# Kernel optimization log

Hardware: AMD Instinct MI355X
Metric: run time of the kernel (lower is better)

Reference implementation:

```python
import jax, jax.numpy as jnp
import numpy as np

H, X, Y = 64, 4, 2
B, N = 64, 4096

def _mlp2(x, W1, b1, W2, b2):
    # GraphEncoderMLP: Linear -> ReLU -> Linear -> ReLU (pointwise over last dim)
    return jax.nn.relu(jnp.dot(jax.nn.relu(jnp.dot(x, W1) + b1), W2) + b2)

def _t(a):
    return jnp.transpose(a, (0, 2, 1))

def _forward(hx, past_curr_mess, fut_curr_mess, y_curr_mess, hy,
             pc_W1, pc_b1, pc_W2, pc_b2,
             fc_W1, fc_b1, fc_W2, fc_b2,
             yc_W1, yc_b1, yc_W2, yc_b2,
             nd_W1, nd_b1, nd_W2, nd_b2,
             W_ih, b_ih, W_hh, b_hh,
             dec_W1, dec_b1, dec_W2, dec_b2):
    # hx: [B, H, N]; messages: [B, X, N]; hy: [B, H, N]
    hx_past = jnp.concatenate([hx[:, :, :1], hx[:, :, :-1]], axis=2)
    hx_fut = jnp.concatenate([hx[:, :, 1:], hx[:, :, -1:]], axis=2)
    pc_in = _t(jnp.concatenate([hx_past, hx, past_curr_mess], axis=1))  # [B,N,2H+X]
    fc_in = _t(jnp.concatenate([hx_fut, hx, fut_curr_mess], axis=1))
    yc_in = _t(jnp.concatenate([hy, hx, y_curr_mess], axis=1))
    pe = _mlp2(pc_in, pc_W1, pc_b1, pc_W2, pc_b2)  # [B,N,H]
    fe = _mlp2(fc_in, fc_W1, fc_b1, fc_W2, fc_b2)
    ye = _mlp2(yc_in, yc_W1, yc_b1, yc_W2, yc_b2)
    U = _mlp2(pe + fe + ye, nd_W1, nd_b1, nd_W2, nd_b2)  # [B,N,H]
    hprev = _t(hx)  # [B,N,H]
    gi = jnp.dot(U, W_ih) + b_ih          # [B,N,3H]
    gh = jnp.dot(hprev, W_hh) + b_hh
    ir, iz, ig = jnp.split(gi, 3, axis=-1)
    hr, hz, hg = jnp.split(gh, 3, axis=-1)
    r = jax.nn.sigmoid(ir + hr)
    z = jax.nn.sigmoid(iz + hz)
    n = jnp.tanh(ig + r * hg)
    hnew = (1.0 - z) * n + z * hprev      # [B,N,H]
    # GraphDecoder: pointwise Linear -> ReLU -> Linear to x_dim
    eps = jnp.dot(jax.nn.relu(jnp.dot(hnew, dec_W1) + dec_b1), dec_W2) + dec_b2  # [B,N,X]
    return _t(eps), _t(hnew)  # ([B,X,N], [B,H,N])

def setup_inputs() -> dict:
    key = jax.random.key(0)
    ks = jax.random.split(key, 40)
    s = 0.05
    d = {
        'hx': jax.random.normal(ks[0], (B, H, N), jnp.float32),
        'past_curr_mess': jax.random.normal(ks[1], (B, X, N), jnp.float32),
        'fut_curr_mess': jax.random.normal(ks[2], (B, X, N), jnp.float32),
        'y_curr_mess': jax.random.normal(ks[3], (B, X, N), jnp.float32),
        'hy': jax.random.normal(ks[4], (B, H, N), jnp.float32),
    }
    i = 5
    for name in ['pc', 'fc', 'yc']:
        d[name + '_W1'] = jax.random.normal(ks[i], (2 * H + X, H), jnp.float32) * s; i += 1
        d[name + '_b1'] = jnp.zeros((H,), jnp.float32)
        d[name + '_W2'] = jax.random.normal(ks[i], (H, H), jnp.float32) * s; i += 1
        d[name + '_b2'] = jnp.zeros((H,), jnp.float32)
    d['nd_W1'] = jax.random.normal(ks[i], (H, H), jnp.float32) * s; i += 1
    d['nd_b1'] = jnp.zeros((H,), jnp.float32)
    d['nd_W2'] = jax.random.normal(ks[i], (H, H), jnp.float32) * s; i += 1
    d['nd_b2'] = jnp.zeros((H,), jnp.float32)
    d['W_ih'] = jax.random.normal(ks[i], (H, 3 * H), jnp.float32) * s; i += 1
    d['b_ih'] = jnp.zeros((3 * H,), jnp.float32)
    d['W_hh'] = jax.random.normal(ks[i], (H, 3 * H), jnp.float32) * s; i += 1
    d['b_hh'] = jnp.zeros((3 * H,), jnp.float32)
    d['dec_W1'] = jax.random.normal(ks[i], (H, H), jnp.float32) * s; i += 1
    d['dec_b1'] = jnp.zeros((H,), jnp.float32)
    d['dec_W2'] = jax.random.normal(ks[i], (H, X), jnp.float32) * s; i += 1
    d['dec_b2'] = jnp.zeros((X,), jnp.float32)
    return d

def reference(hx, past_curr_mess, fut_curr_mess, y_curr_mess, hy,
              pc_W1, pc_b1, pc_W2, pc_b2,
              fc_W1, fc_b1, fc_W2, fc_b2,
              yc_W1, yc_b1, yc_W2, yc_b2,
              nd_W1, nd_b1, nd_W2, nd_b2,
              W_ih, b_ih, W_hh, b_hh,
              dec_W1, dec_b1, dec_W2, dec_b2):
    return _forward(hx, past_curr_mess, fut_curr_mess, y_curr_mess, hy,
                    pc_W1, pc_b1, pc_W2, pc_b2,
                    fc_W1, fc_b1, fc_W2, fc_b2,
                    yc_W1, yc_b1, yc_W2, yc_b2,
                    nd_W1, nd_b1, nd_W2, nd_b2,
                    W_ih, b_ih, W_hh, b_hh,
                    dec_W1, dec_b1, dec_W2, dec_b2)
```

## Files before the change

### kernel.cpp

```cpp
#include <hip/hip_runtime.h>

#define NPOS 4096
#define NB   64

typedef __bf16 bf8v __attribute__((ext_vector_type(8)));
typedef float  f4   __attribute__((ext_vector_type(4)));

__device__ __forceinline__ float sigm(float x)   { return 1.0f / (1.0f + __expf(-x)); }
__device__ __forceinline__ float tanh_f(float x) { return 1.0f - 2.0f / (1.0f + __expf(2.0f * x)); }

__device__ __forceinline__ f4 MF(bf8v a, bf8v b, f4 c) {
    return __builtin_amdgcn_mfma_f32_16x16x32_bf16(a, b, c, 0, 0, 0);
}

__device__ __forceinline__ void gl_lds16(const void* g, void* l) {
    __builtin_amdgcn_global_load_lds(
        (const __attribute__((address_space(1))) void*)g,
        (__attribute__((address_space(3)))       void*)l,
        16, 0, 0);
}

#define NFRAG 211

__global__ __launch_bounds__(64) void prep_kernel(
    const float* __restrict__ pcW1, const float* __restrict__ pcb1, const float* __restrict__ pcW2, const float* __restrict__ pcb2,
    const float* __restrict__ fcW1, const float* __restrict__ fcb1, const float* __restrict__ fcW2, const float* __restrict__ fcb2,
    const float* __restrict__ ycW1, const float* __restrict__ ycb1, const float* __restrict__ ycW2, const float* __restrict__ ycb2,
    const float* __restrict__ ndW1, const float* __restrict__ ndb1, const float* __restrict__ ndW2, const float* __restrict__ ndb2,
    const float* __restrict__ Wih,  const float* __restrict__ bih,  const float* __restrict__ Whh,  const float* __restrict__ bhh,
    const float* __restrict__ dW1,  const float* __restrict__ db1,  const float* __restrict__ dW2,  const float* __restrict__ db2,
    char* __restrict__ ws)
{
    const int f = blockIdx.x, l = threadIdx.x;
    const int sg = l >> 4, c16 = l & 15;
    char* dst = ws + (size_t)f * 1024 + (size_t)l * 16;

    int kind = 0;
    const float* W = nullptr; const float* B1 = nullptr; const float* B2 = nullptr;
    int t = 0, kb = 0, ncol = 64, coloff = 0, boff = 0, mlp = 0;
    bool msgmask = false, decw2 = false, db2frag = false, perm = false;

    if (f < 108) {
        const int m = f / 36, r = f % 36;
        const float* W1 = (m == 0 ? pcW1 : (m == 1 ? fcW1 : ycW1));
        const float* W2 = (m == 0 ? pcW2 : (m == 1 ? fcW2 : ycW2));
        const float* b1 = (m == 0 ? pcb1 : (m == 1 ? fcb1 : ycb1));
        const float* b2 = (m == 0 ? pcb2 : (m == 1 ? fcb2 : ycb2));
        if (r < 20)      { W = W1; kb = r >> 2; t = r & 3; msgmask = (kb == 4); mlp = m; }
        else if (r < 28) { W = W2; int rr = r - 20; kb = rr >> 2; t = rr & 3; perm = true; }
        else if (r < 32) { kind = 1; B1 = b1; t = r - 28; }
        else             { kind = 1; B1 = b2; t = r - 32; }
    } else if (f < 132) {
        const int r = f - 108;
        if (r < 8)       { W = ndW1; kb = r >> 2; t = r & 3; perm = true; }
        else if (r < 16) { W = ndW2; int rr = r - 8; kb = rr >> 2; t = rr & 3; perm = true; }
        else if (r < 20) { kind = 1; B1 = ndb1; t = r - 16; }
        else             { kind = 1; B1 = ndb2; t = r - 20; }
    } else if (f < 164) {
        const int r = f - 132; ncol = 192;
        if (r < 8)       { W = Whh; coloff = 128; kb = r >> 2; t = r & 3; }
        else if (r < 16) { W = Wih; coloff = 0;   int rr = r - 8;  kb = rr >> 2; t = rr & 3; perm = true; }
        else if (r < 24) { W = Whh; coloff = 0;   int rr = r - 16; kb = rr >> 2; t = rr & 3; }
        else if (r < 28) { kind = 1; B1 = bhh; boff = 128; t = r - 24; }
        else             { kind = 1; B1 = bih; B2 = bhh; boff = 0; t = r - 28; }
    } else if (f < 196) {
        const int r = f - 164; ncol = 192;
        if (r < 8)       { W = Wih; coloff = 128; kb = r >> 2; t = r & 3; perm = true; }
        else if (r < 16) { W = Wih; coloff = 64;  int rr = r - 8;  kb = rr >> 2; t = rr & 3; perm = true; }
        else if (r < 24) { W = Whh; coloff = 64;  int rr = r - 16; kb = rr >> 2; t = rr & 3; }
        else if (r < 28) { kind = 1; B1 = bih; boff = 128; t = r - 24; }
        else             { kind = 1; B1 = bih; B2 = bhh; boff = 64; t = r - 28; }
    } else {
        const int r = f - 196;
        if (r < 8)       { W = dW1; kb = r >> 2; t = r & 3; perm = true; }
        else if (r < 10) { W = dW2; kb = r - 8; t = 0; decw2 = true; perm = true; }
        else if (r < 14) { kind = 1; B1 = db1; t = r - 10; }
        else             { kind = 1; B1 = db2; t = 0; db2frag = true; }
    }

    if (!kind) {
        const int row = 16 * t + c16;
        bf8v v;
        #pragma unroll
        for (int j = 0; j < 8; ++j) {
            const int k = perm ? (kb * 32 + 16 * (j >> 2) + 4 * sg + (j & 3))
                               : (kb * 32 + sg * 8 + j);
            float x;
            if (msgmask) { const int kk = k - 128 - mlp * 4; x = (kk >= 0 && kk < 4) ? W[(128 + kk) * 64 + row] : 0.f; }
            else if (decw2) { x = (row < 4) ? W[k * 4 + row] : 0.f; }
            else { x = W[k * ncol + coloff + row]; }
            v[j] = (__bf16)x;
        }
        *(bf8v*)dst = v;
    } else {
        f4 o;
        #pragma unroll
        for (int r4 = 0; r4 < 4; ++r4) {
            float x;
            if (db2frag) { x = (sg == 0 && t == 0) ? B1[r4] : 0.f; }
            else {
                const int fi = boff + 16 * t + 4 * sg + r4;
                x = B1[fi]; if (B2) x += B2[fi];
            }
            o[r4] = x;
        }
        *(f4*)dst = o;
    }
}

#define WSTRIDE 36864
#define LDSZ    73728

__global__ __launch_bounds__(256, 2) void kgnn_main(
    const float* __restrict__ hx,  const float* __restrict__ pcm,
    const float* __restrict__ fcm, const float* __restrict__ ycm,
    const float* __restrict__ hy,
    const char*  __restrict__ ws,  float* __restrict__ out)
{
    __shared__ __align__(16) char LD[LDSZ];
    char* const bufA = LD;
    char* const bufB = LD + WSTRIDE;
    const int tid  = threadIdx.x;
    const int b    = blockIdx.x >> 5;
    const int tile = blockIdx.x & 31;
    const int n0   = tile * 128;
    const int baseH = b * 64 * NPOS;
    const int baseX = b * 4 * NPOS;

    const int lane = tid & 63, wid = tid >> 6;
    const int s = lane >> 4, q = lane & 15;
    const int Pv[2] = { wid * 32 + q, wid * 32 + 16 + q };
    const int Gn[2] = { n0 + Pv[0], n0 + Pv[1] };

    auto ldTB = [&](const float* __restrict__ T, int gnq, int h) -> bf8v {
        bf8v v;
        #pragma unroll
        for (int j = 0; j < 8; ++j)
            v[j] = (__bf16)T[baseH + (h * 32 + 8 * s + j) * NPOS + gnq];
        return v;
    };
    auto packB = [&](const f4* aa, int h, bool relu) -> bf8v {
        bf8v v;
        #pragma unroll
        for (int j = 0; j < 8; ++j) {
            float x = aa[2 * h + (j >> 2)][j & 3];
            if (relu) x = fmaxf(x, 0.f);
            v[j] = (__bf16)x;
        }
        return v;
    };

    bf8v hxn0[2], hxn1[2], msgB[2];
    #pragma unroll
    for (int cc = 0; cc < 2; ++cc) {
        hxn0[cc] = ldTB(hx, Gn[cc], 0);
        hxn1[cc] = ldTB(hx, Gn[cc], 1);
        #pragma unroll
        for (int j = 0; j < 8; ++j) {
            const int idx = 8 * s + j;
            float x = 0.f;
            if      (idx < 4)  x = pcm[baseX + idx * NPOS + Gn[cc]];
            else if (idx < 8)  x = fcm[baseX + (idx - 4) * NPOS + Gn[cc]];
            else if (idx < 12) x = ycm[baseX + (idx - 8) * NPOS + Gn[cc]];
            msgB[cc][j] = (__bf16)x;
        }
    }

    auto stageA = [&](char* dstbuf, int gbase, int nf) {
        #pragma unroll
        for (int f0 = 0; f0 < 9; ++f0) {
            const int f = f0 * 4 + wid;
            if (f < nf)
                gl_lds16(ws + ((size_t)(gbase + f) << 10) + ((size_t)lane << 4),
                         dstbuf + (f << 10));
        }
    };

    auto ldAL = [&](const char* base, int fl) -> bf8v {
        return *(const bf8v*)(base + (fl << 10) + (lane << 4));
    };
    auto ldBiasL = [&](const char* base, int fl) -> f4 {
        return *(const f4*)(base + (fl << 10) + (lane << 4));
    };

    stageA(bufA, 0, 36);
    __syncthreads();

    bf8v sB[2][2];
    #pragma unroll
    for (int m = 0; m < 3; ++m) {
        char* cur = (m & 1) ? bufB : bufA;
        char* oth = (m & 1) ? bufA : bufB;
        stageA(oth, (m == 0) ? 36 : (m == 1 ? 72 : 108), (m == 2) ? 24 : 36);

        bf8v e0[2], e1[2];
        #pragma unroll
        for (int cc = 0; cc < 2; ++cc) {
            if (m == 0) {
                const int gm = (Gn[cc] == 0) ? 0 : Gn[cc] - 1;
                e0[cc] = ldTB(hx, gm, 0); e1[cc] = ldTB(hx, gm, 1);
            } else if (m == 1) {
                const int gp = (Gn[cc] == NPOS - 1) ? NPOS - 1 : Gn[cc] + 1;
                e0[cc] = ldTB(hx, gp, 0); e1[cc] = ldTB(hx, gp, 1);
            } else {
                e0[cc] = ldTB(hy, Gn[cc], 0); e1[cc] = ldTB(hy, Gn[cc], 1);
            }
        }
        f4 a[2][4];
        #pragma unroll
        for (int t = 0; t < 4; ++t) { f4 bv = ldBiasL(cur, 28 + t); a[0][t] = bv; a[1][t] = bv; }
        #pragma unroll
        for (int t = 0; t < 4; ++t) { bf8v A = ldAL(cur, t);      a[0][t] = MF(A, e0[0],   a[0][t]); a[1][t] = MF(A, e0[1],   a[1][t]); }
        #pragma unroll
        for (int t = 0; t < 4; ++t) { bf8v A = ldAL(cur, 4 + t);  a[0][t] = MF(A, e1[0],   a[0][t]); a[1][t] = MF(A, e1[1],   a[1][t]); }
        #pragma unroll
        for (int t = 0; t < 4; ++t) { bf8v A = ldAL(cur, 8 + t);  a[0][t] = MF(A, hxn0[0], a[0][t]); a[1][t] = MF(A, hxn0[1], a[1][t]); }
        #pragma unroll
        for (int t = 0; t < 4; ++t) { bf8v A = ldAL(cur, 12 + t); a[0][t] = MF(A, hxn1[0], a[0][t]); a[1][t] = MF(A, hxn1[1], a[1][t]); }
        #pragma unroll
        for (int t = 0; t < 4; ++t) { bf8v A = ldAL(cur, 16 + t); a[0][t] = MF(A, msgB[0], a[0][t]); a[1][t] = MF(A, msgB[1], a[1][t]); }

        bf8v u0[2] = { packB(a[0], 0, true), packB(a[1], 0, true) };
        bf8v u1[2] = { packB(a[0], 1, true), packB(a[1], 1, true) };

        f4 a2[2][4];
        #pragma unroll
        for (int t = 0; t < 4; ++t) { f4 bv = ldBiasL(cur, 32 + t); a2[0][t] = bv; a2[1][t] = bv; }
        #pragma unroll
        for (int t = 0; t < 4; ++t) { bf8v A = ldAL(cur, 20 + t); a2[0][t] = MF(A, u0[0], a2[0][t]); a2[1][t] = MF(A, u0[1], a2[1][t]); }
        #pragma unroll
        for (int t = 0; t < 4; ++t) { bf8v A = ldAL(cur, 24 + t); a2[0][t] = MF(A, u1[0], a2[0][t]); a2[1][t] = MF(A, u1[1], a2[1][t]); }
        #pragma unroll
        for (int cc = 0; cc < 2; ++cc)
            #pragma unroll
            for (int h = 0; h < 2; ++h) {
                bf8v p = packB(a2[cc], h, true);
                if (m == 0) sB[cc][h] = p;
                else {
                    #pragma unroll
                    for (int j = 0; j < 8; ++j)
                        sB[cc][h][j] = (__bf16)((float)sB[cc][h][j] + (float)p[j]);
                }
            }
        __syncthreads();
    }

    bf8v uu0[2], uu1[2];
    {
        stageA(bufA, 132, 32);
        f4 a[2][4];
        #pragma unroll
        for (int t = 0; t < 4; ++t) { f4 bv = ldBiasL(bufB, 16 + t); a[0][t] = bv; a[1][t] = bv; }
        #pragma unroll
        for (int t = 0; t < 4; ++t) { bf8v A = ldAL(bufB, t);     a[0][t] = MF(A, sB[0][0], a[0][t]); a[1][t] = MF(A, sB[1][0], a[1][t]); }
        #pragma unroll
        for (int t = 0; t < 4; ++t) { bf8v A = ldAL(bufB, 4 + t); a[0][t] = MF(A, sB[0][1], a[0][t]); a[1][t] = MF(A, sB[1][1], a[1][t]); }
        bf8v w0[2] = { packB(a[0], 0, true), packB(a[1], 0, true) };
        bf8v w1[2] = { packB(a[0], 1, true), packB(a[1], 1, true) };
        f4 a2[2][4];
        #pragma unroll
        for (int t = 0; t < 4; ++t) { f4 bv = ldBiasL(bufB, 20 + t); a2[0][t] = bv; a2[1][t] = bv; }
        #pragma unroll
        for (int t = 0; t < 4; ++t) { bf8v A = ldAL(bufB, 8 + t);  a2[0][t] = MF(A, w0[0], a2[0][t]); a2[1][t] = MF(A, w0[1], a2[1][t]); }
        #pragma unroll
        for (int t = 0; t < 4; ++t) { bf8v A = ldAL(bufB, 12 + t); a2[0][t] = MF(A, w1[0], a2[0][t]); a2[1][t] = MF(A, w1[1], a2[1][t]); }
        uu0[0] = packB(a2[0], 0, true); uu0[1] = packB(a2[1], 0, true);
        uu1[0] = packB(a2[0], 1, true); uu1[1] = packB(a2[1], 1, true);
        __syncthreads();
    }

    bf8v gB[2][2];
    {
        stageA(bufB, 164, 32);
        f4 g0[2][4];
        #pragma unroll
        for (int t = 0; t < 4; ++t) { f4 bv = ldBiasL(bufA, 24 + t); g0[0][t] = bv; g0[1][t] = bv; }
        #pragma unroll
        for (int t = 0; t < 4; ++t) { bf8v A = ldAL(bufA, t);     g0[0][t] = MF(A, hxn0[0], g0[0][t]); g0[1][t] = MF(A, hxn0[1], g0[1][t]); }
        #pragma unroll
        for (int t = 0; t < 4; ++t) { bf8v A = ldAL(bufA, 4 + t); g0[0][t] = MF(A, hxn1[0], g0[0][t]); g0[1][t] = MF(A, hxn1[1], g0[1][t]); }
        f4 rr[2][4];
        #pragma unroll
        for (int t = 0; t < 4; ++t) { f4 bv = ldBiasL(bufA, 28 + t); rr[0][t] = bv; rr[1][t] = bv; }
        #pragma unroll
        for (int t = 0; t < 4; ++t) { bf8v A = ldAL(bufA, 8 + t);  rr[0][t] = MF(A, uu0[0], rr[0][t]); rr[1][t] = MF(A, uu0[1], rr[1][t]); }
        #pragma unroll
        for (int t = 0; t < 4; ++t) { bf8v A = ldAL(bufA, 12 + t); rr[0][t] = MF(A, uu1[0], rr[0][t]); rr[1][t] = MF(A, uu1[1], rr[1][t]); }
        #pragma unroll
        for (int t = 0; t < 4; ++t) { bf8v A = ldAL(bufA, 16 + t); rr[0][t] = MF(A, hxn0[0], rr[0][t]); rr[1][t] = MF(A, hxn0[1], rr[1][t]); }
        #pragma unroll
        for (int t = 0; t < 4; ++t) { bf8v A = ldAL(bufA, 20 + t); rr[0][t] = MF(A, hxn1[0], rr[0][t]); rr[1][t] = MF(A, hxn1[1], rr[1][t]); }
        #pragma unroll
        for (int cc = 0; cc < 2; ++cc)
            #pragma unroll
            for (int t = 0; t < 4; ++t)
                #pragma unroll
                for (int r = 0; r < 4; ++r)
                    gB[cc][t >> 1][(t & 1) * 4 + r] = (__bf16)(sigm(rr[cc][t][r]) * g0[cc][t][r]);
        __syncthreads();
    }

    bf8v hnB0[2], hnB1[2];
    {
        stageA(bufA, 196, 15);
        f4 gi[2][4];
        #pragma unroll
        for (int t = 0; t < 4; ++t) { f4 bv = ldBiasL(bufB, 24 + t); gi[0][t] = bv; gi[1][t] = bv; }
        #pragma unroll
        for (int t = 0; t < 4; ++t) { bf8v A = ldAL(bufB, t);     gi[0][t] = MF(A, uu0[0], gi[0][t]); gi[1][t] = MF(A, uu0[1], gi[1][t]); }
        #pragma unroll
        for (int t = 0; t < 4; ++t) { bf8v A = ldAL(bufB, 4 + t); gi[0][t] = MF(A, uu1[0], gi[0][t]); gi[1][t] = MF(A, uu1[1], gi[1][t]); }
        bf8v nB[2][2];
        #pragma unroll
        for (int cc = 0; cc < 2; ++cc)
            #pragma unroll
            for (int t = 0; t < 4; ++t)
                #pragma unroll
                for (int r = 0; r < 4; ++r)
                    nB[cc][t >> 1][(t & 1) * 4 + r] =
                        (__bf16)tanh_f(gi[cc][t][r] + (float)gB[cc][t >> 1][(t & 1) * 4 + r]);

        f4 hpv[2][4];
        #pragma unroll
        for (int cc = 0; cc < 2; ++cc)
            #pragma unroll
            for (int t = 0; t < 4; ++t)
                #pragma unroll
                for (int r = 0; r < 4; ++r)
                    hpv[cc][t][r] = hx[baseH + (16 * t + 4 * s + r) * NPOS + Gn[cc]];

        f4 zz[2][4];
        #pragma unroll
        for (int t = 0; t < 4; ++t) { f4 bv = ldBiasL(bufB, 28 + t); zz[0][t] = bv; zz[1][t] = bv; }
        #pragma unroll
        for (int t = 0; t < 4; ++t) { bf8v A = ldAL(bufB, 8 + t);  zz[0][t] = MF(A, uu0[0], zz[0][t]); zz[1][t] = MF(A, uu0[1], zz[1][t]); }
        #pragma unroll
        for (int t = 0; t < 4; ++t) { bf8v A = ldAL(bufB, 12 + t); zz[0][t] = MF(A, uu1[0], zz[0][t]); zz[1][t] = MF(A, uu1[1], zz[1][t]); }
        #pragma unroll
        for (int t = 0; t < 4; ++t) { bf8v A = ldAL(bufB, 16 + t); zz[0][t] = MF(A, hxn0[0], zz[0][t]); zz[1][t] = MF(A, hxn0[1], zz[1][t]); }
        #pragma unroll
        for (int t = 0; t < 4; ++t) { bf8v A = ldAL(bufB, 20 + t); zz[0][t] = MF(A, hxn1[0], zz[0][t]); zz[1][t] = MF(A, hxn1[1], zz[1][t]); }

        float* __restrict__ outH = out + NB * 4 * NPOS + baseH;
        #pragma unroll
        for (int cc = 0; cc < 2; ++cc)
            #pragma unroll
            for (int t = 0; t < 4; ++t)
                #pragma unroll
                for (int r = 0; r < 4; ++r) {
                    float z  = sigm(zz[cc][t][r]);
                    float nn = (float)nB[cc][t >> 1][(t & 1) * 4 + r];
                    float hv = nn + z * (hpv[cc][t][r] - nn);
                    outH[(16 * t + 4 * s + r) * NPOS + Gn[cc]] = hv;
                    if (t < 2) hnB0[cc][(t & 1) * 4 + r] = (__bf16)hv;
                    else       hnB1[cc][(t & 1) * 4 + r] = (__bf16)hv;
                }
        __syncthreads();
    }

    {
        f4 a[2][4];
        #pragma unroll
        for (int t = 0; t < 4; ++t) { f4 bv = ldBiasL(bufA, 10 + t); a[0][t] = bv; a[1][t] = bv; }
        #pragma unroll
        for (int t = 0; t < 4; ++t) { bf8v A = ldAL(bufA, t);     a[0][t] = MF(A, hnB0[0], a[0][t]); a[1][t] = MF(A, hnB0[1], a[1][t]); }
        #pragma unroll
        for (int t = 0; t < 4; ++t) { bf8v A = ldAL(bufA, 4 + t); a[0][t] = MF(A, hnB1[0], a[0][t]); a[1][t] = MF(A, hnB1[1], a[1][t]); }
        bf8v e0[2] = { packB(a[0], 0, true), packB(a[1], 0, true) };
        bf8v e1[2] = { packB(a[0], 1, true), packB(a[1], 1, true) };
        f4 ep[2];
        { f4 bv = ldBiasL(bufA, 14); ep[0] = bv; ep[1] = bv; }
        { bf8v A = ldAL(bufA, 8); ep[0] = MF(A, e0[0], ep[0]); ep[1] = MF(A, e0[1], ep[1]); }
        { bf8v A = ldAL(bufA, 9); ep[0] = MF(A, e1[0], ep[0]); ep[1] = MF(A, e1[1], ep[1]); }
        if (s == 0) {
            #pragma unroll
            for (int cc = 0; cc < 2; ++cc) {
                #pragma unroll
                for (int r = 0; r < 4; ++r) out[baseX + r * NPOS + Gn[cc]] = ep[cc][r];
            }
        }
    }
}

extern "C" void kernel_launch(void* const* d_in, const int* in_sizes, int n_in,
                              void* d_out, int out_size, void* d_ws, size_t ws_size,
                              hipStream_t stream) {
    const float* hx   = (const float*)d_in[0];
    const float* pcm  = (const float*)d_in[1];
    const float* fcm  = (const float*)d_in[2];
    const float* ycm  = (const float*)d_in[3];
    const float* hy   = (const float*)d_in[4];

    prep_kernel<<<dim3(NFRAG), dim3(64), 0, stream>>>(
        (const float*)d_in[5],  (const float*)d_in[6],  (const float*)d_in[7],  (const float*)d_in[8],
        (const float*)d_in[9],  (const float*)d_in[10], (const float*)d_in[11], (const float*)d_in[12],
        (const float*)d_in[13], (const float*)d_in[14], (const float*)d_in[15], (const float*)d_in[16],
        (const float*)d_in[17], (const float*)d_in[18], (const float*)d_in[19], (const float*)d_in[20],
        (const float*)d_in[21], (const float*)d_in[22], (const float*)d_in[23], (const float*)d_in[24],
        (const float*)d_in[25], (const float*)d_in[26], (const float*)d_in[27], (const float*)d_in[28],
        (char*)d_ws);

    kgnn_main<<<dim3(NB * 32), dim3(256), 0, stream>>>(
        hx, pcm, fcm, ycm, hy, (const char*)d_ws, (float*)d_out);
}
```

Baseline: 100.4 us.

## Split block work across 8 waves with one 16-column chunk per wave

Each block now launches 512 threads (8 waves) instead of 256, and each wave handles a single 16-position column group instead of two. This halves per-thread register state (accumulators, B fragments) and doubles the waves available for latency hiding, while the LDS weight staging is spread across 8 waves. Each weight fragment loaded from LDS now feeds only one MFMA instead of two, so LDS read traffic per MFMA doubles. The launch bounds request 4 blocks per CU, which the 72KB of LDS per block may not permit.

```diff
diff --git a/kernel.cpp b/kernel.cpp
--- a/kernel.cpp
+++ b/kernel.cpp
@@ -111,7 +111,7 @@
 #define WSTRIDE 36864
 #define LDSZ    73728
 
-__global__ __launch_bounds__(256, 2) void kgnn_main(
+__global__ __launch_bounds__(512, 4) void kgnn_main(
     const float* __restrict__ hx,  const float* __restrict__ pcm,
     const float* __restrict__ fcm, const float* __restrict__ ycm,
     const float* __restrict__ hy,
@@ -129,8 +129,8 @@
 
     const int lane = tid & 63, wid = tid >> 6;
     const int s = lane >> 4, q = lane & 15;
-    const int Pv[2] = { wid * 32 + q, wid * 32 + 16 + q };
-    const int Gn[2] = { n0 + Pv[0], n0 + Pv[1] };
+    const int Pv = wid * 16 + q;
+    const int Gn = n0 + Pv;
 
     auto ldTB = [&](const float* __restrict__ T, int gnq, int h) -> bf8v {
         bf8v v;
@@ -150,26 +150,23 @@
         return v;
     };
 
-    bf8v hxn0[2], hxn1[2], msgB[2];
+    bf8v hxn0 = ldTB(hx, Gn, 0);
+    bf8v hxn1 = ldTB(hx, Gn, 1);
+    bf8v msgB;
     #pragma unroll
-    for (int cc = 0; cc < 2; ++cc) {
-        hxn0[cc] = ldTB(hx, Gn[cc], 0);
-        hxn1[cc] = ldTB(hx, Gn[cc], 1);
-        #pragma unroll
-        for (int j = 0; j < 8; ++j) {
-            const int idx = 8 * s + j;
-            float x = 0.f;
-            if      (idx < 4)  x = pcm[baseX + idx * NPOS + Gn[cc]];
-            else if (idx < 8)  x = fcm[baseX + (idx - 4) * NPOS + Gn[cc]];
-            else if (idx < 12) x = ycm[baseX + (idx - 8) * NPOS + Gn[cc]];
-            msgB[cc][j] = (__bf16)x;
-        }
+    for (int j = 0; j < 8; ++j) {
+        const int idx = 8 * s + j;
+        float x = 0.f;
+        if      (idx < 4)  x = pcm[baseX + idx * NPOS + Gn];
+        else if (idx < 8)  x = fcm[baseX + (idx - 4) * NPOS + Gn];
+        else if (idx < 12) x = ycm[baseX + (idx - 8) * NPOS + Gn];
+        msgB[j] = (__bf16)x;
     }
 
     auto stageA = [&](char* dstbuf, int gbase, int nf) {
         #pragma unroll
-        for (int f0 = 0; f0 < 9; ++f0) {
-            const int f = f0 * 4 + wid;
+        for (int f0 = 0; f0 < 5; ++f0) {
+            const int f = f0 * 8 + wid;
             if (f < nf)
                 gl_lds16(ws + ((size_t)(gbase + f) << 10) + ((size_t)lane << 4),
                          dstbuf + (f << 10));
@@ -186,198 +183,188 @@
     stageA(bufA, 0, 36);
     __syncthreads();
 
-    bf8v sB[2][2];
+    bf8v sB[2];
     #pragma unroll
     for (int m = 0; m < 3; ++m) {
         char* cur = (m & 1) ? bufB : bufA;
         char* oth = (m & 1) ? bufA : bufB;
         stageA(oth, (m == 0) ? 36 : (m == 1 ? 72 : 108), (m == 2) ? 24 : 36);
 
-        bf8v e0[2], e1[2];
-        #pragma unroll
-        for (int cc = 0; cc < 2; ++cc) {
-            if (m == 0) {
-                const int gm = (Gn[cc] == 0) ? 0 : Gn[cc] - 1;
-                e0[cc] = ldTB(hx, gm, 0); e1[cc] = ldTB(hx, gm, 1);
-            } else if (m == 1) {
-                const int gp = (Gn[cc] == NPOS - 1) ? NPOS - 1 : Gn[cc] + 1;
-                e0[cc] = ldTB(hx, gp, 0); e1[cc] = ldTB(hx, gp, 1);
-            } else {
-                e0[cc] = ldTB(hy, Gn[cc], 0); e1[cc] = ldTB(hy, Gn[cc], 1);
-            }
-        }
-        f4 a[2][4];
-        #pragma unroll
-        for (int t = 0; t < 4; ++t) { f4 bv = ldBiasL(cur, 28 + t); a[0][t] = bv; a[1][t] = bv; }
-        #pragma unroll
-        for (int t = 0; t < 4; ++t) { bf8v A = ldAL(cur, t);      a[0][t] = MF(A, e0[0],   a[0][t]); a[1][t] = MF(A, e0[1],   a[1][t]); }
-        #pragma unroll
-        for (int t = 0; t < 4; ++t) { bf8v A = ldAL(cur, 4 + t);  a[0][t] = MF(A, e1[0],   a[0][t]); a[1][t] = MF(A, e1[1],   a[1][t]); }
-        #pragma unroll
-        for (int t = 0; t < 4; ++t) { bf8v A = ldAL(cur, 8 + t);  a[0][t] = MF(A, hxn0[0], a[0][t]); a[1][t] = MF(A, hxn0[1], a[1][t]); }
-        #pragma unroll
-        for (int t = 0; t < 4; ++t) { bf8v A = ldAL(cur, 12 + t); a[0][t] = MF(A, hxn1[0], a[0][t]); a[1][t] = MF(A, hxn1[1], a[1][t]); }
-        #pragma unroll
-        for (int t = 0; t < 4; ++t) { bf8v A = ldAL(cur, 16 + t); a[0][t] = MF(A, msgB[0], a[0][t]); a[1][t] = MF(A, msgB[1], a[1][t]); }
-
-        bf8v u0[2] = { packB(a[0], 0, true), packB(a[1], 0, true) };
-        bf8v u1[2] = { packB(a[0], 1, true), packB(a[1], 1, true) };
-
-        f4 a2[2][4];
-        #pragma unroll
-        for (int t = 0; t < 4; ++t) { f4 bv = ldBiasL(cur, 32 + t); a2[0][t] = bv; a2[1][t] = bv; }
-        #pragma unroll
-        for (int t = 0; t < 4; ++t) { bf8v A = ldAL(cur, 20 + t); a2[0][t] = MF(A, u0[0], a2[0][t]); a2[1][t] = MF(A, u0[1], a2[1][t]); }
-        #pragma unroll
-        for (int t = 0; t < 4; ++t) { bf8v A = ldAL(cur, 24 + t); a2[0][t] = MF(A, u1[0], a2[0][t]); a2[1][t] = MF(A, u1[1], a2[1][t]); }
-        #pragma unroll
-        for (int cc = 0; cc < 2; ++cc)
-            #pragma unroll
-            for (int h = 0; h < 2; ++h) {
-                bf8v p = packB(a2[cc], h, true);
-                if (m == 0) sB[cc][h] = p;
-                else {
-                    #pragma unroll
-                    for (int j = 0; j < 8; ++j)
-                        sB[cc][h][j] = (__bf16)((float)sB[cc][h][j] + (float)p[j]);
-                }
-            }
+        bf8v e0, e1;
+        if (m == 0) {
+            const int gm = (Gn == 0) ? 0 : Gn - 1;
+            e0 = ldTB(hx, gm, 0); e1 = ldTB(hx, gm, 1);
+        } else if (m == 1) {
+            const int gp = (Gn == NPOS - 1) ? NPOS - 1 : Gn + 1;
+            e0 = ldTB(hx, gp, 0); e1 = ldTB(hx, gp, 1);
+        } else {
+            e0 = ldTB(hy, Gn, 0); e1 = ldTB(hy, Gn, 1);
+        }
+        f4 a[4];
+        #pragma unroll
+        for (int t = 0; t < 4; ++t) a[t] = ldBiasL(cur, 28 + t);
+        #pragma unroll
+        for (int t = 0; t < 4; ++t) a[t] = MF(ldAL(cur, t),      e0,   a[t]);
+        #pragma unroll
+        for (int t = 0; t < 4; ++t) a[t] = MF(ldAL(cur, 4 + t),  e1,   a[t]);
+        #pragma unroll
+        for (int t = 0; t < 4; ++t) a[t] = MF(ldAL(cur, 8 + t),  hxn0, a[t]);
+        #pragma unroll
+        for (int t = 0; t < 4; ++t) a[t] = MF(ldAL(cur, 12 + t), hxn1, a[t]);
+        #pragma unroll
+        for (int t = 0; t < 4; ++t) a[t] = MF(ldAL(cur, 16 + t), msgB, a[t]);
+
+        bf8v u0 = packB(a, 0, true);
+        bf8v u1 = packB(a, 1, true);
+
+        f4 a2[4];
+        #pragma unroll
+        for (int t = 0; t < 4; ++t) a2[t] = ldBiasL(cur, 32 + t);
+        #pragma unroll
+        for (int t = 0; t < 4; ++t) a2[t] = MF(ldAL(cur, 20 + t), u0, a2[t]);
+        #pragma unroll
+        for (int t = 0; t < 4; ++t) a2[t] = MF(ldAL(cur, 24 + t), u1, a2[t]);
+        #pragma unroll
+        for (int h = 0; h < 2; ++h) {
+            bf8v p = packB(a2, h, true);
+            if (m == 0) sB[h] = p;
+            else {
+                #pragma unroll
+                for (int j = 0; j < 8; ++j)
+                    sB[h][j] = (__bf16)((float)sB[h][j] + (float)p[j]);
+            }
+        }
         __syncthreads();
     }
 
-    bf8v uu0[2], uu1[2];
+    bf8v uu0, uu1;
     {
         stageA(bufA, 132, 32);
-        f4 a[2][4];
-        #pragma unroll
-        for (int t = 0; t < 4; ++t) { f4 bv = ldBiasL(bufB, 16 + t); a[0][t] = bv; a[1][t] = bv; }
-        #pragma unroll
-        for (int t = 0; t < 4; ++t) { bf8v A = ldAL(bufB, t);     a[0][t] = MF(A, sB[0][0], a[0][t]); a[1][t] = MF(A, sB[1][0], a[1][t]); }
-        #pragma unroll
-        for (int t = 0; t < 4; ++t) { bf8v A = ldAL(bufB, 4 + t); a[0][t] = MF(A, sB[0][1], a[0][t]); a[1][t] = MF(A, sB[1][1], a[1][t]); }
-        bf8v w0[2] = { packB(a[0], 0, true), packB(a[1], 0, true) };
-        bf8v w1[2] = { packB(a[0], 1, true), packB(a[1], 1, true) };
-        f4 a2[2][4];
-        #pragma unroll
-        for (int t = 0; t < 4; ++t) { f4 bv = ldBiasL(bufB, 20 + t); a2[0][t] = bv; a2[1][t] = bv; }
-        #pragma unroll
-        for (int t = 0; t < 4; ++t) { bf8v A = ldAL(bufB, 8 + t);  a2[0][t] = MF(A, w0[0], a2[0][t]); a2[1][t] = MF(A, w0[1], a2[1][t]); }
-        #pragma unroll
-        for (int t = 0; t < 4; ++t) { bf8v A = ldAL(bufB, 12 + t); a2[0][t] = MF(A, w1[0], a2[0][t]); a2[1][t] = MF(A, w1[1], a2[1][t]); }
-        uu0[0] = packB(a2[0], 0, true); uu0[1] = packB(a2[1], 0, true);
-        uu1[0] = packB(a2[0], 1, true); uu1[1] = packB(a2[1], 1, true);
+        f4 a[4];
+        #pragma unroll
+        for (int t = 0; t < 4; ++t) a[t] = ldBiasL(bufB, 16 + t);
+        #pragma unroll
+        for (int t = 0; t < 4; ++t) a[t] = MF(ldAL(bufB, t),     sB[0], a[t]);
+        #pragma unroll
+        for (int t = 0; t < 4; ++t) a[t] = MF(ldAL(bufB, 4 + t), sB[1], a[t]);
+        bf8v w0 = packB(a, 0, true);
+        bf8v w1 = packB(a, 1, true);
+        f4 a2[4];
+        #pragma unroll
+        for (int t = 0; t < 4; ++t) a2[t] = ldBiasL(bufB, 20 + t);
+        #pragma unroll
+        for (int t = 0; t < 4; ++t) a2[t] = MF(ldAL(bufB, 8 + t),  w0, a2[t]);
+        #pragma unroll
+        for (int t = 0; t < 4; ++t) a2[t] = MF(ldAL(bufB, 12 + t), w1, a2[t]);
+        uu0 = packB(a2, 0, true);
+        uu1 = packB(a2, 1, true);
         __syncthreads();
     }
 
-    bf8v gB[2][2];
+    bf8v gB;
+    bf8v gB2;
     {
         stageA(bufB, 164, 32);
-        f4 g0[2][4];
-        #pragma unroll
-        for (int t = 0; t < 4; ++t) { f4 bv = ldBiasL(bufA, 24 + t); g0[0][t] = bv; g0[1][t] = bv; }
-        #pragma unroll
-        for (int t = 0; t < 4; ++t) { bf8v A = ldAL(bufA, t);     g0[0][t] = MF(A, hxn0[0], g0[0][t]); g0[1][t] = MF(A, hxn0[1], g0[1][t]); }
-        #pragma unroll
-        for (int t = 0; t < 4; ++t) { bf8v A = ldAL(bufA, 4 + t); g0[0][t] = MF(A, hxn1[0], g0[0][t]); g0[1][t] = MF(A, hxn1[1], g0[1][t]); }
-        f4 rr[2][4];
-        #pragma unroll
-        for (int t = 0; t < 4; ++t) { f4 bv = ldBiasL(bufA, 28 + t); rr[0][t] = bv; rr[1][t] = bv; }
-        #pragma unroll
-        for (int t = 0; t < 4; ++t) { bf8v A = ldAL(bufA, 8 + t);  rr[0][t] = MF(A, uu0[0], rr[0][t]); rr[1][t] = MF(A, uu0[1], rr[1][t]); }
-        #pragma unroll
-        for (int t = 0; t < 4; ++t) { bf8v A = ldAL(bufA, 12 + t); rr[0][t] = MF(A, uu1[0], rr[0][t]); rr[1][t] = MF(A, uu1[1], rr[1][t]); }
-        #pragma unroll
-        for (int t = 0; t < 4; ++t) { bf8v A = ldAL(bufA, 16 + t); rr[0][t] = MF(A, hxn0[0], rr[0][t]); rr[1][t] = MF(A, hxn0[1], rr[1][t]); }
-        #pragma unroll
-        for (int t = 0; t < 4; ++t) { bf8v A = ldAL(bufA, 20 + t); rr[0][t] = MF(A, hxn1[0], rr[0][t]); rr[1][t] = MF(A, hxn1[1], rr[1][t]); }
-        #pragma unroll
-        for (int cc = 0; cc < 2; ++cc)
-            #pragma unroll
-            for (int t = 0; t < 4; ++t)
-                #pragma unroll
-                for (int r = 0; r < 4; ++r)
-                    gB[cc][t >> 1][(t & 1) * 4 + r] = (__bf16)(sigm(rr[cc][t][r]) * g0[cc][t][r]);
+        f4 g0[4];
+        #pragma unroll
+        for (int t = 0; t < 4; ++t) g0[t] = ldBiasL(bufA, 24 + t);
+        #pragma unroll
+        for (int t = 0; t < 4; ++t) g0[t] = MF(ldAL(bufA, t),     hxn0, g0[t]);
+        #pragma unroll
+        for (int t = 0; t < 4; ++t) g0[t] = MF(ldAL(bufA, 4 + t), hxn1, g0[t]);
+        f4 rr[4];
+        #pragma unroll
+        for (int t = 0; t < 4; ++t) rr[t] = ldBiasL(bufA, 28 + t);
+        #pragma unroll
+        for (int t = 0; t < 4; ++t) rr[t] = MF(ldAL(bufA, 8 + t),  uu0,  rr[t]);
+        #pragma unroll
+        for (int t = 0; t < 4; ++t) rr[t] = MF(ldAL(bufA, 12 + t), uu1,  rr[t]);
+        #pragma unroll
+        for (int t = 0; t < 4; ++t) rr[t] = MF(ldAL(bufA, 16 + t), hxn0, rr[t]);
+        #pragma unroll
+        for (int t = 0; t < 4; ++t) rr[t] = MF(ldAL(bufA, 20 + t), hxn1, rr[t]);
+        #pragma unroll
+        for (int t = 0; t < 4; ++t)
+            #pragma unroll
+            for (int r = 0; r < 4; ++r) {
+                float v = sigm(rr[t][r]) * g0[t][r];
+                if (t < 2) gB[(t & 1) * 4 + r]  = (__bf16)v;
+                else       gB2[(t & 1) * 4 + r] = (__bf16)v;
+            }
         __syncthreads();
     }
 
-    bf8v hnB0[2], hnB1[2];
+    bf8v hnB0, hnB1;
     {
         stageA(bufA, 196, 15);
-        f4 gi[2][4];
-        #pragma unroll
-        for (int t = 0; t < 4; ++t) { f4 bv = ldBiasL(bufB, 24 + t); gi[0][t] = bv; gi[1][t] = bv; }
-        #pragma unroll
-        for (int t = 0; t < 4; ++t) { bf8v A = ldAL(bufB, t);     gi[0][t] = MF(A, uu0[0], gi[0][t]); gi[1][t] = MF(A, uu0[1], gi[1][t]); }
-        #pragma unroll
-        for (int t = 0; t < 4; ++t) { bf8v A = ldAL(bufB, 4 + t); gi[0][t] = MF(A, uu1[0], gi[0][t]); gi[1][t] = MF(A, uu1[1], gi[1][t]); }
-        bf8v nB[2][2];
-        #pragma unroll
-        for (int cc = 0; cc < 2; ++cc)
-            #pragma unroll
-            for (int t = 0; t < 4; ++t)
-                #pragma unroll
-                for (int r = 0; r < 4; ++r)
-                    nB[cc][t >> 1][(t & 1) * 4 + r] =
-                        (__bf16)tanh_f(gi[cc][t][r] + (float)gB[cc][t >> 1][(t & 1) * 4 + r]);
-
-        f4 hpv[2][4];
-        #pragma unroll
-        for (int cc = 0; cc < 2; ++cc)
-            #pragma unroll
-            for (int t = 0; t < 4; ++t)
-                #pragma unroll
-                for (int r = 0; r < 4; ++r)
-                    hpv[cc][t][r] = hx[baseH + (16 * t + 4 * s + r) * NPOS + Gn[cc]];
-
-        f4 zz[2][4];
-        #pragma unroll
-        for (int t = 0; t < 4; ++t) { f4 bv = ldBiasL(bufB, 28 + t); zz[0][t] = bv; zz[1][t] = bv; }
-        #pragma unroll
-        for (int t = 0; t < 4; ++t) { bf8v A = ldAL(bufB, 8 + t);  zz[0][t] = MF(A, uu0[0], zz[0][t]); zz[1][t] = MF(A, uu0[1], zz[1][t]); }
-        #pragma unroll
-        for (int t = 0; t < 4; ++t) { bf8v A = ldAL(bufB, 12 + t); zz[0][t] = MF(A, uu1[0], zz[0][t]); zz[1][t] = MF(A, uu1[1], zz[1][t]); }
-        #pragma unroll
-        for (int t = 0; t < 4; ++t) { bf8v A = ldAL(bufB, 16 + t); zz[0][t] = MF(A, hxn0[0], zz[0][t]); zz[1][t] = MF(A, hxn0[1], zz[1][t]); }
-        #pragma unroll
-        for (int t = 0; t < 4; ++t) { bf8v A = ldAL(bufB, 20 + t); zz[0][t] = MF(A, hxn1[0], zz[0][t]); zz[1][t] = MF(A, hxn1[1], zz[1][t]); }
+        f4 gi[4];
+        #pragma unroll
+        for (int t = 0; t < 4; ++t) gi[t] = ldBiasL(bufB, 24 + t);
+        #pragma unroll
+        for (int t = 0; t < 4; ++t) gi[t] = MF(ldAL(bufB, t),     uu0, gi[t]);
+        #pragma unroll
+        for (int t = 0; t < 4; ++t) gi[t] = MF(ldAL(bufB, 4 + t), uu1, gi[t]);
+        bf8v nB0, nB1;
+        #pragma unroll
+        for (int t = 0; t < 4; ++t)
+            #pragma unroll
+            for (int r = 0; r < 4; ++r) {
+                float gv = (t < 2) ? (float)gB[(t & 1) * 4 + r] : (float)gB2[(t & 1) * 4 + r];
+                float v = tanh_f(gi[t][r] + gv);
+                if (t < 2) nB0[(t & 1) * 4 + r] = (__bf16)v;
+                else       nB1[(t & 1) * 4 + r] = (__bf16)v;
+            }
+
+        f4 hpv[4];
+        #pragma unroll
+        for (int t = 0; t < 4; ++t)
+            #pragma unroll
+            for (int r = 0; r < 4; ++r)
+                hpv[t][r] = hx[baseH + (16 * t + 4 * s + r) * NPOS + Gn];
+
+        f4 zz[4];
+        #pragma unroll
+        for (int t = 0; t < 4; ++t) zz[t] = ldBiasL(bufB, 28 + t);
+        #pragma unroll
+        for (int t = 0; t < 4; ++t) zz[t] = MF(ldAL(bufB, 8 + t),  uu0,  zz[t]);
+        #pragma unroll
+        for (int t = 0; t < 4; ++t) zz[t] = MF(ldAL(bufB, 12 + t), uu1,  zz[t]);
+        #pragma unroll
+        for (int t = 0; t < 4; ++t) zz[t] = MF(ldAL(bufB, 16 + t), hxn0, zz[t]);
+        #pragma unroll
+        for (int t = 0; t < 4; ++t) zz[t] = MF(ldAL(bufB, 20 + t), hxn1, zz[t]);
 
         float* __restrict__ outH = out + NB * 4 * NPOS + baseH;
         #pragma unroll
-        for (int cc = 0; cc < 2; ++cc)
-            #pragma unroll
-            for (int t = 0; t < 4; ++t)
-                #pragma unroll
-                for (int r = 0; r < 4; ++r) {
-                    float z  = sigm(zz[cc][t][r]);
-                    float nn = (float)nB[cc][t >> 1][(t & 1) * 4 + r];
-                    float hv = nn + z * (hpv[cc][t][r] - nn);
-                    outH[(16 * t + 4 * s + r) * NPOS + Gn[cc]] = hv;
-                    if (t < 2) hnB0[cc][(t & 1) * 4 + r] = (__bf16)hv;
-                    else       hnB1[cc][(t & 1) * 4 + r] = (__bf16)hv;
-                }
+        for (int t = 0; t < 4; ++t)
+            #pragma unroll
+            for (int r = 0; r < 4; ++r) {
+                float z  = sigm(zz[t][r]);
+                float nn = (t < 2) ? (float)nB0[(t & 1) * 4 + r] : (float)nB1[(t & 1) * 4 + r];
+                float hv = nn + z * (hpv[t][r] - nn);
+                outH[(16 * t + 4 * s + r) * NPOS + Gn] = hv;
+                if (t < 2) hnB0[(t & 1) * 4 + r] = (__bf16)hv;
+                else       hnB1[(t & 1) * 4 + r] = (__bf16)hv;
+            }
         __syncthreads();
     }
 
     {
-        f4 a[2][4];
-        #pragma unroll
-        for (int t = 0; t < 4; ++t) { f4 bv = ldBiasL(bufA, 10 + t); a[0][t] = bv; a[1][t] = bv; }
-        #pragma unroll
-        for (int t = 0; t < 4; ++t) { bf8v A = ldAL(bufA, t);     a[0][t] = MF(A, hnB0[0], a[0][t]); a[1][t] = MF(A, hnB0[1], a[1][t]); }
-        #pragma unroll
-        for (int t = 0; t < 4; ++t) { bf8v A = ldAL(bufA, 4 + t); a[0][t] = MF(A, hnB1[0], a[0][t]); a[1][t] = MF(A, hnB1[1], a[1][t]); }
-        bf8v e0[2] = { packB(a[0], 0, true), packB(a[1], 0, true) };
-        bf8v e1[2] = { packB(a[0], 1, true), packB(a[1], 1, true) };
-        f4 ep[2];
-        { f4 bv = ldBiasL(bufA, 14); ep[0] = bv; ep[1] = bv; }
-        { bf8v A = ldAL(bufA, 8); ep[0] = MF(A, e0[0], ep[0]); ep[1] = MF(A, e0[1], ep[1]); }
-        { bf8v A = ldAL(bufA, 9); ep[0] = MF(A, e1[0], ep[0]); ep[1] = MF(A, e1[1], ep[1]); }
+        f4 a[4];
+        #pragma unroll
+        for (int t = 0; t < 4; ++t) a[t] = ldBiasL(bufA, 10 + t);
+        #pragma unroll
+        for (int t = 0; t < 4; ++t) a[t] = MF(ldAL(bufA, t),     hnB0, a[t]);
+        #pragma unroll
+        for (int t = 0; t < 4; ++t) a[t] = MF(ldAL(bufA, 4 + t), hnB1, a[t]);
+        bf8v e0 = packB(a, 0, true);
+        bf8v e1 = packB(a, 1, true);
+        f4 ep = ldBiasL(bufA, 14);
+        ep = MF(ldAL(bufA, 8), e0, ep);
+        ep = MF(ldAL(bufA, 9), e1, ep);
         if (s == 0) {
             #pragma unroll
-            for (int cc = 0; cc < 2; ++cc) {
-                #pragma unroll
-                for (int r = 0; r < 4; ++r) out[baseX + r * NPOS + Gn[cc]] = ep[cc][r];
-            }
+            for (int r = 0; r < 4; ++r) out[baseX + r * NPOS + Gn] = ep[r];
         }
     }
 }
@@ -400,6 +387,6 @@
         (const float*)d_in[25], (const float*)d_in[26], (const float*)d_in[27], (const float*)d_in[28],
         (char*)d_ws);
 
-    kgnn_main<<<dim3(NB * 32), dim3(256), 0, stream>>>(
+    kgnn_main<<<dim3(NB * 32), dim3(512), 0, stream>>>(
         hx, pcm, fcm, ycm, hy, (const char*)d_ws, (float*)d_out);
 }
```

After: 93.13 us. 1.08x faster.
